# Kernel tuning notes

Hardware: AMD Instinct MI355X
Metric: run time of the kernel (lower is better)

## Reference

```python
import jax, jax.numpy as jnp
import numpy as np

B, J, D, W, H, EH, L = 128, 8192, 32, 4, 128, 256, 32
TEMP = 1.0


def _ln(x, g, b, eps=1e-5):
    mu = jnp.mean(x, axis=-1, keepdims=True)
    var = jnp.var(x, axis=-1, keepdims=True)
    return (x - mu) * jax.lax.rsqrt(var + eps) * g + b


def setup_inputs() -> dict:
    key = jax.random.key(0)
    ks = jax.random.split(key, 12)

    def lin(k, fi, fo):
        k1, k2 = jax.random.split(k)
        s = 1.0 / np.sqrt(fi)
        return (jax.random.uniform(k1, (fi, fo), minval=-s, maxval=s, dtype=jnp.float32),
                jax.random.uniform(k2, (fo,), minval=-s, maxval=s, dtype=jnp.float32))

    h_w1, h_b1 = lin(ks[0], 1 + D, H)
    h_w2, h_b2 = lin(ks[1], H, D)
    g_w1, g_b1 = lin(ks[2], D, D // 2)
    g_w2, g_b2 = lin(ks[3], D // 2, W)
    c_w, c_b = lin(ks[4], W * D, D)
    e_w1, e_b1 = lin(ks[5], D, EH)
    e_w2, e_b2 = lin(ks[6], EH, 2 * L)
    return {
        'x': jax.random.normal(ks[7], (B, J), dtype=jnp.float32),
        'mask': jax.random.randint(ks[8], (B, J), 0, 2, dtype=jnp.int32),
        'fe': jax.random.normal(ks[9], (J, D), dtype=jnp.float32),
        'h_w1': h_w1, 'h_b1': h_b1,
        'h_ln1_w': jnp.ones((H,), jnp.float32), 'h_ln1_b': jnp.zeros((H,), jnp.float32),
        'h_w2': h_w2, 'h_b2': h_b2,
        'h_ln2_w': jnp.ones((D,), jnp.float32), 'h_ln2_b': jnp.zeros((D,), jnp.float32),
        'g_w1': g_w1, 'g_b1': g_b1, 'g_w2': g_w2, 'g_b2': g_b2,
        'c_w': c_w, 'c_b': c_b,
        'c_ln_w': jnp.ones((D,), jnp.float32), 'c_ln_b': jnp.zeros((D,), jnp.float32),
        'e_w1': e_w1, 'e_b1': e_b1,
        'e_ln1_w': jnp.ones((EH,), jnp.float32), 'e_ln1_b': jnp.zeros((EH,), jnp.float32),
        'e_w2': e_w2, 'e_b2': e_b2,
        'e_ln2_w': jnp.ones((2 * L,), jnp.float32), 'e_ln2_b': jnp.zeros((2 * L,), jnp.float32),
    }


def _forward(x, mask, fe, h_w1, h_b1, h_ln1_w, h_ln1_b, h_w2, h_b2, h_ln2_w, h_ln2_b,
             g_w1, g_b1, g_w2, g_b2, c_w, c_b, c_ln_w, c_ln_b,
             e_w1, e_b1, e_ln1_w, e_ln1_b, e_w2, e_b2, e_ln2_w, e_ln2_b):
    relu = jax.nn.relu
    # h_in = concat([x, F]) @ h_w1 split into scalar column + shared embedding part
    # (fe @ h_w1[1:]) is [J,H], shared across cells -> avoids materializing [B,J,1+D]
    pre = x[..., None] * h_w1[0][None, None, :] + (fe @ h_w1[1:])[None] + h_b1  # [B,J,H]
    h1 = relu(_ln(pre, h_ln1_w, h_ln1_b))
    h_out = relu(_ln(h1 @ h_w2 + h_b2, h_ln2_w, h_ln2_b))  # [B,J,D]
    raw_gates = relu(h_out @ g_w1 + g_b1) @ g_w2 + g_b2  # [B,J,W]
    logits = jnp.clip(raw_gates * TEMP, -10.0, 10.0)
    logits = jnp.where(mask[..., None] > 0, logits, -1e9)  # masked gather -> -inf fill
    weights = jax.nn.softmax(logits, axis=1)  # softmax over observed junctions
    head_sums = jnp.einsum('bjw,bjd->bwd', weights, h_out)  # [B,W,D]
    comb = relu(_ln(head_sums.reshape(head_sums.shape[0], -1) @ c_w + c_b, c_ln_w, c_ln_b))
    comb = jnp.where((jnp.sum(mask, axis=1) > 0)[:, None], comb, 0.0)  # zero cells -> zeros
    h = relu(_ln(comb @ e_w1 + e_b1, e_ln1_w, e_ln1_b))
    o = relu(_ln(h @ e_w2 + e_b2, e_ln2_w, e_ln2_b))
    mu, logvar = jnp.split(o, 2, axis=-1)
    return mu, logvar


def reference(x, mask, fe, h_w1, h_b1, h_ln1_w, h_ln1_b, h_w2, h_b2, h_ln2_w, h_ln2_b,
              g_w1, g_b1, g_w2, g_b2, c_w, c_b, c_ln_w, c_ln_b,
              e_w1, e_b1, e_ln1_w, e_ln1_b, e_w2, e_b2, e_ln2_w, e_ln2_b):
    return _forward(x, mask, fe, h_w1, h_b1, h_ln1_w, h_ln1_b, h_w2, h_b2, h_ln2_w, h_ln2_b,
                    g_w1, g_b1, g_w2, g_b2, c_w, c_b, c_ln_w, c_ln_b,
                    e_w1, e_b1, e_ln1_w, e_ln1_b, e_w2, e_b2, e_ln2_w, e_ln2_b)
```

## Files before the change

kernel.cpp:

```cpp
#include <hip/hip_runtime.h>
#include <cstdint>

#define BDIM 128
#define JDIM 8192

typedef short s8x __attribute__((ext_vector_type(8)));
typedef float f4x __attribute__((ext_vector_type(4)));

__device__ __forceinline__ unsigned int rne16(float f) {
    unsigned int u = __float_as_uint(f);
    return (u + 0x7fffu + ((u >> 16) & 1u)) >> 16;
}
__device__ __forceinline__ unsigned int pkbf(float lo, float hi) {
    return rne16(lo) | (rne16(hi) << 16);
}
__device__ __forceinline__ float bf2f(unsigned int s) {
    return __uint_as_float(s << 16);
}

template <int CTRL>
__device__ __forceinline__ float dppadd(float x) {
    int y = __builtin_amdgcn_update_dpp(0, __builtin_bit_cast(int, x), CTRL, 0xF, 0xF, true);
    return x + __builtin_bit_cast(float, y);
}
__device__ __forceinline__ float allred16(float x) {
    x = dppadd<0xB1>(x);
    x = dppadd<0x4E>(x);
    x = dppadd<0x141>(x);
    x = dppadd<0x140>(x);
    return x;
}

__global__ __launch_bounds__(128) void k_prep(
    const float* __restrict__ fe, const float* __restrict__ hw1,
    const float* __restrict__ hb1,
    unsigned short* __restrict__ feWb, float* __restrict__ aux,
    float* __restrict__ scal)
{
    const int j = blockIdx.x, h = threadIdx.x;
    float acc = hb1[h];
#pragma unroll
    for (int d = 0; d < 32; ++d)
        acc = fmaf(fe[j * 32 + d], hw1[(1 + d) * 128 + h], acc);
    feWb[(size_t)j * 128 + h] = (unsigned short)rne16(acc);

    const float w0h = hw1[h];
    float s1 = acc, sx = w0h * acc, s2 = acc * acc;
#pragma unroll
    for (int m = 1; m <= 32; m <<= 1) {
        s1 += __shfl_xor(s1, m); sx += __shfl_xor(sx, m); s2 += __shfl_xor(s2, m);
    }
    __shared__ float red[2][3];
    const int wv = threadIdx.x >> 6, ln = threadIdx.x & 63;
    if (ln == 0) { red[wv][0] = s1; red[wv][1] = sx; red[wv][2] = s2; }
    __syncthreads();
    if (threadIdx.x == 0) {
        aux[j * 4 + 0] = (red[0][0] + red[1][0]) * (1.f / 128.f);
        aux[j * 4 + 1] = (red[0][1] + red[1][1]) * (1.f / 128.f);
        aux[j * 4 + 2] = (red[0][2] + red[1][2]) * (1.f / 128.f);
    }
    if (j == 0) {
        float a = w0h, b = w0h * w0h;
#pragma unroll
        for (int m = 1; m <= 32; m <<= 1) { a += __shfl_xor(a, m); b += __shfl_xor(b, m); }
        __syncthreads();
        if (ln == 0) { red[wv][0] = a; red[wv][1] = b; }
        __syncthreads();
        if (threadIdx.x == 0) {
            scal[0] = (red[0][0] + red[1][0]) * (1.f / 128.f);
            scal[1] = (red[0][1] + red[1][1]) * (1.f / 128.f);
        }
    }
}

__global__ __launch_bounds__(256, 2) void k_main(
    const float* __restrict__ x, const int* __restrict__ mask,
    const unsigned short* __restrict__ feWb, const float* __restrict__ aux,
    const float* __restrict__ scal,
    const float* __restrict__ hw1, const float* __restrict__ ln1w,
    const float* __restrict__ ln1b,
    const float* __restrict__ hw2, const float* __restrict__ hb2,
    const float* __restrict__ ln2w, const float* __restrict__ ln2b,
    const float* __restrict__ gw1, const float* __restrict__ gb1,
    const float* __restrict__ gw2, const float* __restrict__ gb2,
    float* __restrict__ P, float* __restrict__ SEb, int njb, int jpw)
{
    __shared__ float w0s[128], g1s[128], b1s[128];
    __shared__ float holds[8][576];
    __shared__ float hsL[2048];
    __shared__ float seL[64];

    const int tid = threadIdx.x, l = tid & 63;
    const int wv = __builtin_amdgcn_readfirstlane(tid >> 6);
    const int c = l & 15, g = l >> 4;
    const int bt = blockIdx.y, bx = blockIdx.x;
    const int b0 = bt * 16;

    if (tid < 128) { w0s[tid] = hw1[tid]; g1s[tid] = ln1w[tid]; b1s[tid] = ln1b[tid]; }
    __syncthreads();

    const float mw0 = scal[0], q0 = scal[1];

    s8x wf[2][4];
#pragma unroll
    for (int nt = 0; nt < 2; ++nt)
#pragma unroll
        for (int t = 0; t < 4; ++t) {
            const int kb = 32 * t + 8 * g, n = 16 * nt + c;
            uint4 u;
            u.x = pkbf(hw2[(kb + 0) * 32 + n], hw2[(kb + 1) * 32 + n]);
            u.y = pkbf(hw2[(kb + 2) * 32 + n], hw2[(kb + 3) * 32 + n]);
            u.z = pkbf(hw2[(kb + 4) * 32 + n], hw2[(kb + 5) * 32 + n]);
            u.w = pkbf(hw2[(kb + 6) * 32 + n], hw2[(kb + 7) * 32 + n]);
            wf[nt][t] = __builtin_bit_cast(s8x, u);
        }
    s8x g1f;
    {
        uint4 u;
        u.x = pkbf(gw1[(8 * g + 0) * 16 + c], gw1[(8 * g + 1) * 16 + c]);
        u.y = pkbf(gw1[(8 * g + 2) * 16 + c], gw1[(8 * g + 3) * 16 + c]);
        u.z = pkbf(gw1[(8 * g + 4) * 16 + c], gw1[(8 * g + 5) * 16 + c]);
        u.w = pkbf(gw1[(8 * g + 6) * 16 + c], gw1[(8 * g + 7) * 16 + c]);
        g1f = __builtin_bit_cast(s8x, u);
    }
    const float hb2a = hb2[c],      hb2b = hb2[16 + c];
    const float g2a  = ln2w[c],     g2b  = ln2w[16 + c];
    const float z2a  = ln2b[c],     z2b  = ln2b[16 + c];
    const float gb1c = gb1[c];
    float gw2c[4], gb2v[4];
#pragma unroll
    for (int w = 0; w < 4; ++w) { gw2c[w] = gw2[c * 4 + w]; gb2v[w] = gb2[w]; }

    const int j0 = (bx * 4 + wv) * jpw;
    const float* xrow = x + (size_t)(b0 + c) * JDIM;
    const int*   mrow = mask + (size_t)(b0 + c) * JDIM;

    float hsacc[4][4][2];
    float seacc[4][4];
#pragma unroll
    for (int r = 0; r < 4; ++r)
#pragma unroll
        for (int w = 0; w < 4; ++w) {
            hsacc[r][w][0] = 0.f; hsacc[r][w][1] = 0.f; seacc[r][w] = 0.f;
        }

    for (int jj = 0; jj < jpw; ++jj) {
        const int j = j0 + jj;
        const float xv = xrow[j];
        const int   mv = mrow[j];
        const float4 au = *(const float4*)(aux + j * 4);
        const float m1 = au.x, qx = au.y, q2 = au.z;
        const float mu = fmaf(xv, mw0, m1);
        const float e2 = fmaf(xv * xv, q0, fmaf(2.f * xv, qx, q2));
        const float rs = rsqrtf(e2 - mu * mu + 1e-5f);
        const float nms = -mu * rs;

        f4x ca = {0.f, 0.f, 0.f, 0.f}, cbv = {0.f, 0.f, 0.f, 0.f};
        const unsigned short* fj = feWb + (size_t)j * 128;
#pragma unroll
        for (int t = 0; t < 4; ++t) {
            const int kb = 32 * t + 8 * g;
            const uint4 fw = *(const uint4*)(fj + kb);
            const float pf0 = bf2f(fw.x & 0xffffu), pf1 = bf2f(fw.x >> 16);
            const float pf2 = bf2f(fw.y & 0xffffu), pf3 = bf2f(fw.y >> 16);
            const float pf4 = bf2f(fw.z & 0xffffu), pf5 = bf2f(fw.z >> 16);
            const float pf6 = bf2f(fw.w & 0xffffu), pf7 = bf2f(fw.w >> 16);
            const float4 wa = *(const float4*)&w0s[kb];
            const float4 wb = *(const float4*)&w0s[kb + 4];
            const float4 ga = *(const float4*)&g1s[kb];
            const float4 gbq = *(const float4*)&g1s[kb + 4];
            const float4 ba = *(const float4*)&b1s[kb];
            const float4 bb = *(const float4*)&b1s[kb + 4];
            const float h0 = fmaxf(fmaf(fmaf(fmaf(xv, wa.x, pf0), rs, nms), ga.x,  ba.x), 0.f);
            const float h1 = fmaxf(fmaf(fmaf(fmaf(xv, wa.y, pf1), rs, nms), ga.y,  ba.y), 0.f);
            const float h2 = fmaxf(fmaf(fmaf(fmaf(xv, wa.z, pf2), rs, nms), ga.z,  ba.z), 0.f);
            const float h3 = fmaxf(fmaf(fmaf(fmaf(xv, wa.w, pf3), rs, nms), ga.w,  ba.w), 0.f);
            const float h4 = fmaxf(fmaf(fmaf(fmaf(xv, wb.x, pf4), rs, nms), gbq.x, bb.x), 0.f);
            const float h5 = fmaxf(fmaf(fmaf(fmaf(xv, wb.y, pf5), rs, nms), gbq.y, bb.y), 0.f);
            const float h6 = fmaxf(fmaf(fmaf(fmaf(xv, wb.z, pf6), rs, nms), gbq.z, bb.z), 0.f);
            const float h7 = fmaxf(fmaf(fmaf(fmaf(xv, wb.w, pf7), rs, nms), gbq.w, bb.w), 0.f);
            uint4 u;
            u.x = pkbf(h0, h1); u.y = pkbf(h2, h3); u.z = pkbf(h4, h5); u.w = pkbf(h6, h7);
            const s8x af = __builtin_bit_cast(s8x, u);
            ca  = __builtin_amdgcn_mfma_f32_16x16x32_bf16(af, wf[0][t], ca,  0, 0, 0);
            cbv = __builtin_amdgcn_mfma_f32_16x16x32_bf16(af, wf[1][t], cbv, 0, 0, 0);
        }

        float v0[4], v1[4], sr[4], qr[4];
#pragma unroll
        for (int r = 0; r < 4; ++r) {
            v0[r] = ca[r] + hb2a;
            v1[r] = cbv[r] + hb2b;
            sr[r] = v0[r] + v1[r];
            qr[r] = v0[r] * v0[r] + v1[r] * v1[r];
        }
#pragma unroll
        for (int r = 0; r < 4; ++r) { sr[r] = allred16(sr[r]); qr[r] = allred16(qr[r]); }
        float ho0[4], ho1[4];
#pragma unroll
        for (int r = 0; r < 4; ++r) {
            const float m2  = sr[r] * 0.03125f;
            const float rs2 = rsqrtf(fmaf(qr[r], 0.03125f, -m2 * m2) + 1e-5f);
            const float nm2 = -m2 * rs2;
            ho0[r] = fmaxf(fmaf(fmaf(v0[r], rs2, nm2), g2a, z2a), 0.f);
            ho1[r] = fmaxf(fmaf(fmaf(v1[r], rs2, nm2), g2b, z2b), 0.f);
        }

        float* hp = &holds[wv * 2 + (jj & 1)][0];
#pragma unroll
        for (int r = 0; r < 4; ++r) {
            hp[(4 * g + r) * 36 + c]      = ho0[r];
            hp[(4 * g + r) * 36 + 16 + c] = ho1[r];
        }
        asm volatile("s_waitcnt lgkmcnt(0)" ::: "memory");
        const float4 ra  = *(const float4*)&hp[c * 36 + 8 * g];
        const float4 rb2 = *(const float4*)&hp[c * 36 + 8 * g + 4];
        uint4 ua;
        ua.x = pkbf(ra.x, ra.y);  ua.y = pkbf(ra.z, ra.w);
        ua.z = pkbf(rb2.x, rb2.y); ua.w = pkbf(rb2.z, rb2.w);
        const s8x af2 = __builtin_bit_cast(s8x, ua);
        f4x gc = {0.f, 0.f, 0.f, 0.f};
        gc = __builtin_amdgcn_mfma_f32_16x16x32_bf16(af2, g1f, gc, 0, 0, 0);

        float pw[16];
#pragma unroll
        for (int r = 0; r < 4; ++r) {
            const float g1r = fmaxf(gc[r] + gb1c, 0.f);
#pragma unroll
            for (int w = 0; w < 4; ++w) pw[r * 4 + w] = g1r * gw2c[w];
        }
#pragma unroll
        for (int i = 0; i < 16; ++i) pw[i] = allred16(pw[i]);

        const unsigned bm = (unsigned)__ballot(mv > 0);
        float fm[4];
#pragma unroll
        for (int r = 0; r < 4; ++r) fm[r] = (float)((bm >> (4 * g + r)) & 1u);

#pragma unroll
        for (int r = 0; r < 4; ++r)
#pragma unroll
            for (int w = 0; w < 4; ++w) {
                const float lg = fminf(fmaxf(pw[r * 4 + w] + gb2v[w], -10.f), 10.f);
                const float e  = fm[r] * __builtin_amdgcn_exp2f(
                                     fmaf(lg, 1.44269504089f, -14.4269504089f));
                seacc[r][w] += e;
                hsacc[r][w][0] = fmaf(e, ho0[r], hsacc[r][w][0]);
                hsacc[r][w][1] = fmaf(e, ho1[r], hsacc[r][w][1]);
            }
    }

    for (int ww = 0; ww < 4; ++ww) {
        __syncthreads();
        if (wv == ww) {
#pragma unroll
            for (int r = 0; r < 4; ++r)
#pragma unroll
                for (int w = 0; w < 4; ++w)
#pragma unroll
                    for (int nt = 0; nt < 2; ++nt) {
                        const int idx = ((4 * g + r) * 4 + w) * 32 + c + 16 * nt;
                        if (ww == 0) hsL[idx] = hsacc[r][w][nt];
                        else         hsL[idx] += hsacc[r][w][nt];
                    }
            if (c == 0) {
#pragma unroll
                for (int r = 0; r < 4; ++r)
#pragma unroll
                    for (int w = 0; w < 4; ++w) {
                        const int si = (4 * g + r) * 4 + w;
                        if (ww == 0) seL[si] = seacc[r][w];
                        else         seL[si] += seacc[r][w];
                    }
            }
        }
    }
    __syncthreads();
    const size_t base = ((size_t)bt * njb + bx) * 2048;
    for (int i = tid; i < 2048; i += 256) P[base + i] = hsL[i];
    if (tid < 64) SEb[((size_t)bt * njb + bx) * 64 + tid] = seL[tid];
}

__global__ __launch_bounds__(128) void k_tail(
    const float* __restrict__ P, const float* __restrict__ SEb,
    const float* __restrict__ cw, const float* __restrict__ cbv,
    const float* __restrict__ clnw, const float* __restrict__ clnb,
    const float* __restrict__ ew1, const float* __restrict__ eb1,
    const float* __restrict__ l1w, const float* __restrict__ l1b,
    const float* __restrict__ ew2, const float* __restrict__ eb2,
    const float* __restrict__ l2w, const float* __restrict__ l2b,
    float* __restrict__ out, int njb)
{
    const int b = blockIdx.x, t = threadIdx.x;
    const int bt = b >> 4, bi = b & 15;
    __shared__ float hsLs[128], combL[32], hL[256], seW[4], sred[64], red[4];

    const float* Pb = P + (size_t)bt * njb * 2048 + bi * 128;
    float sacc = 0.f;
#pragma unroll 4
    for (int jc = 0; jc < njb; ++jc) sacc += Pb[(size_t)jc * 2048 + t];

    if (t < 64) {
        const int w = t & 3, part = t >> 2;
        float sp = 0.f;
        for (int q = part; q < njb; q += 16)
            sp += SEb[((size_t)bt * njb + q) * 64 + bi * 4 + w];
        sred[t] = sp;
    }
    __syncthreads();
    if (t < 4) {
        float v = 0.f;
#pragma unroll
        for (int sl = 0; sl < 16; ++sl) v += sred[sl * 4 + t];
        seW[t] = v;
    }
    __syncthreads();
    const bool has = seW[0] > 0.f;
    hsLs[t] = has ? sacc / seW[t >> 5] : 0.f;
    __syncthreads();

    if (t < 32) {
        float cv = cbv[t];
#pragma unroll 4
        for (int f = 0; f < 128; ++f) cv = fmaf(hsLs[f], cw[f * 32 + t], cv);
        float s = cv, q = cv * cv;
#pragma unroll
        for (int m = 1; m <= 16; m <<= 1) { s += __shfl_xor(s, m); q += __shfl_xor(q, m); }
        const float mu = s * (1.f / 32.f);
        const float rsg = rsqrtf(fmaf(q, 1.f / 32.f, -mu * mu) + 1e-5f);
        const float v = fmaf(fmaf(cv, rsg, -mu * rsg), clnw[t], clnb[t]);
        combL[t] = has ? fmaxf(v, 0.f) : 0.f;
    }
    __syncthreads();

    float h0 = eb1[t], h1v = eb1[t + 128];
#pragma unroll 4
    for (int d = 0; d < 32; ++d) {
        const float cd = combL[d];
        h0  = fmaf(cd, ew1[d * 256 + t], h0);
        h1v = fmaf(cd, ew1[d * 256 + t + 128], h1v);
    }
    {
        float s = h0 + h1v, q = h0 * h0 + h1v * h1v;
#pragma unroll
        for (int m = 1; m <= 32; m <<= 1) { s += __shfl_xor(s, m); q += __shfl_xor(q, m); }
        const int wv = t >> 6, ln = t & 63;
        if (ln == 0) { red[wv * 2] = s; red[wv * 2 + 1] = q; }
    }
    __syncthreads();
    {
        const float S = red[0] + red[2], Q = red[1] + red[3];
        const float mu1 = S * (1.f / 256.f);
        const float rs1 = rsqrtf(fmaf(Q, 1.f / 256.f, -mu1 * mu1) + 1e-5f);
        hL[t]       = fmaxf(fmaf(fmaf(h0,  rs1, -mu1 * rs1), l1w[t],       l1b[t]),       0.f);
        hL[t + 128] = fmaxf(fmaf(fmaf(h1v, rs1, -mu1 * rs1), l1w[t + 128], l1b[t + 128]), 0.f);
    }
    __syncthreads();

    if (t < 64) {
        float ov = eb2[t];
#pragma unroll 4
        for (int m = 0; m < 256; ++m) ov = fmaf(hL[m], ew2[m * 64 + t], ov);
        float s = ov, q = ov * ov;
#pragma unroll
        for (int m = 1; m <= 32; m <<= 1) { s += __shfl_xor(s, m); q += __shfl_xor(q, m); }
        const float mu2 = s * (1.f / 64.f);
        const float rs2 = rsqrtf(fmaf(q, 1.f / 64.f, -mu2 * mu2) + 1e-5f);
        const float o = fmaxf(fmaf(fmaf(ov, rs2, -mu2 * rs2), l2w[t], l2b[t]), 0.f);
        if (t < 32) out[b * 32 + t] = o;
        else        out[4096 + b * 32 + (t - 32)] = o;
    }
}

extern "C" void kernel_launch(void* const* d_in, const int* in_sizes, int n_in,
                              void* d_out, int out_size, void* d_ws, size_t ws_size,
                              hipStream_t stream)
{
    (void)in_sizes; (void)n_in; (void)out_size;
    const float* x    = (const float*)d_in[0];
    const int*   mask = (const int*)d_in[1];
    const float* fe   = (const float*)d_in[2];
    const float* hw1  = (const float*)d_in[3];
    const float* hb1  = (const float*)d_in[4];
    const float* ln1w = (const float*)d_in[5];
    const float* ln1b = (const float*)d_in[6];
    const float* hw2  = (const float*)d_in[7];
    const float* hb2  = (const float*)d_in[8];
    const float* ln2w = (const float*)d_in[9];
    const float* ln2b = (const float*)d_in[10];
    const float* gw1  = (const float*)d_in[11];
    const float* gb1  = (const float*)d_in[12];
    const float* gw2  = (const float*)d_in[13];
    const float* gb2  = (const float*)d_in[14];
    const float* cw   = (const float*)d_in[15];
    const float* cbv  = (const float*)d_in[16];
    const float* clnw = (const float*)d_in[17];
    const float* clnb = (const float*)d_in[18];
    const float* ew1  = (const float*)d_in[19];
    const float* eb1  = (const float*)d_in[20];
    const float* l1w  = (const float*)d_in[21];
    const float* l1b  = (const float*)d_in[22];
    const float* ew2  = (const float*)d_in[23];
    const float* eb2  = (const float*)d_in[24];
    const float* l2w  = (const float*)d_in[25];
    const float* l2b  = (const float*)d_in[26];

    const size_t base = (2u << 20) + (128u << 10) + 256u;
    int NJB = 128;
    {
        const size_t need = base + (size_t)8 * 128 * 2048 * 4 + (size_t)8 * 128 * 64 * 4;
        if (ws_size < need) NJB = 64;
    }
    const int JPW = JDIM / (NJB * 4);

    char* ws = (char*)d_ws;
    unsigned short* feWb = (unsigned short*)ws;
    float* aux  = (float*)(ws + (2u << 20));
    float* scal = (float*)(ws + (2u << 20) + (128u << 10));
    float* P    = (float*)(ws + base);
    float* SEb  = (float*)(ws + base + (size_t)8 * NJB * 2048 * 4);

    hipLaunchKernelGGL(k_prep, dim3(JDIM), dim3(128), 0, stream,
                       fe, hw1, hb1, feWb, aux, scal);
    hipLaunchKernelGGL(k_main, dim3(NJB, 8), dim3(256), 0, stream,
                       x, mask, feWb, aux, scal,
                       hw1, ln1w, ln1b, hw2, hb2, ln2w, ln2b,
                       gw1, gb1, gw2, gb2, P, SEb, NJB, JPW);
    hipLaunchKernelGGL(k_tail, dim3(BDIM), dim3(128), 0, stream,
                       P, SEb, cw, cbv, clnw, clnb,
                       ew1, eb1, l1w, l1b, ew2, eb2, l2w, l2b,
                       (float*)d_out, NJB);
}
```

Baseline: 256.3 us.

## Use LDS atomics for cross-wave reduction, raise J-block count, and use hardware bf16 conversion

Replaces the serialized four-step wave-by-wave LDS accumulation with zero-initialized shared buffers and LDS atomicAdd, which removes three barriers. It also swaps the manual round-to-nearest bf16 conversion for the compiler's __bf16 cast, and replaces the fmin/fmax clamp with fmed3. NJB grows to 256 when the workspace allows, doubling the grid, and the tail kernel's partial-sum loop unrolls further. The extra blocks mean more partials for k_tail to reduce, and the atomic accumulation can contend on LDS.

```diff
diff --git a/kernel.cpp b/kernel.cpp
--- a/kernel.cpp
+++ b/kernel.cpp
@@ -7,12 +7,11 @@
 typedef short s8x __attribute__((ext_vector_type(8)));
 typedef float f4x __attribute__((ext_vector_type(4)));
 
-__device__ __forceinline__ unsigned int rne16(float f) {
-    unsigned int u = __float_as_uint(f);
-    return (u + 0x7fffu + ((u >> 16) & 1u)) >> 16;
+__device__ __forceinline__ unsigned short bf16u(float f) {
+    return __builtin_bit_cast(unsigned short, (__bf16)f);
 }
 __device__ __forceinline__ unsigned int pkbf(float lo, float hi) {
-    return rne16(lo) | (rne16(hi) << 16);
+    return (unsigned int)bf16u(lo) | ((unsigned int)bf16u(hi) << 16);
 }
 __device__ __forceinline__ float bf2f(unsigned int s) {
     return __uint_as_float(s << 16);
@@ -42,7 +41,7 @@
 #pragma unroll
     for (int d = 0; d < 32; ++d)
         acc = fmaf(fe[j * 32 + d], hw1[(1 + d) * 128 + h], acc);
-    feWb[(size_t)j * 128 + h] = (unsigned short)rne16(acc);
+    feWb[(size_t)j * 128 + h] = bf16u(acc);
 
     const float w0h = hw1[h];
     float s1 = acc, sx = w0h * acc, s2 = acc * acc;
@@ -97,6 +96,8 @@
     const int b0 = bt * 16;
 
     if (tid < 128) { w0s[tid] = hw1[tid]; g1s[tid] = ln1w[tid]; b1s[tid] = ln1b[tid]; }
+    for (int i = tid; i < 2048; i += 256) hsL[i] = 0.f;
+    if (tid < 64) seL[tid] = 0.f;
     __syncthreads();
 
     const float mw0 = scal[0], q0 = scal[1];
@@ -241,7 +242,7 @@
         for (int r = 0; r < 4; ++r)
 #pragma unroll
             for (int w = 0; w < 4; ++w) {
-                const float lg = fminf(fmaxf(pw[r * 4 + w] + gb2v[w], -10.f), 10.f);
+                const float lg = __builtin_amdgcn_fmed3f(pw[r * 4 + w] + gb2v[w], -10.f, 10.f);
                 const float e  = fm[r] * __builtin_amdgcn_exp2f(
                                      fmaf(lg, 1.44269504089f, -14.4269504089f));
                 seacc[r][w] += e;
@@ -250,31 +251,18 @@
             }
     }
 
-    for (int ww = 0; ww < 4; ++ww) {
-        __syncthreads();
-        if (wv == ww) {
-#pragma unroll
-            for (int r = 0; r < 4; ++r)
-#pragma unroll
-                for (int w = 0; w < 4; ++w)
-#pragma unroll
-                    for (int nt = 0; nt < 2; ++nt) {
-                        const int idx = ((4 * g + r) * 4 + w) * 32 + c + 16 * nt;
-                        if (ww == 0) hsL[idx] = hsacc[r][w][nt];
-                        else         hsL[idx] += hsacc[r][w][nt];
-                    }
-            if (c == 0) {
-#pragma unroll
-                for (int r = 0; r < 4; ++r)
-#pragma unroll
-                    for (int w = 0; w < 4; ++w) {
-                        const int si = (4 * g + r) * 4 + w;
-                        if (ww == 0) seL[si] = seacc[r][w];
-                        else         seL[si] += seacc[r][w];
-                    }
+    __syncthreads();
+#pragma unroll
+    for (int r = 0; r < 4; ++r)
+#pragma unroll
+        for (int w = 0; w < 4; ++w) {
+#pragma unroll
+            for (int nt = 0; nt < 2; ++nt) {
+                const int idx = ((4 * g + r) * 4 + w) * 32 + c + 16 * nt;
+                atomicAdd(&hsL[idx], hsacc[r][w][nt]);
             }
-        }
-    }
+            if (c == 0) atomicAdd(&seL[(4 * g + r) * 4 + w], seacc[r][w]);
+        }
     __syncthreads();
     const size_t base = ((size_t)bt * njb + bx) * 2048;
     for (int i = tid; i < 2048; i += 256) P[base + i] = hsL[i];
@@ -297,7 +285,7 @@
 
     const float* Pb = P + (size_t)bt * njb * 2048 + bi * 128;
     float sacc = 0.f;
-#pragma unroll 4
+#pragma unroll 8
     for (int jc = 0; jc < njb; ++jc) sacc += Pb[(size_t)jc * 2048 + t];
 
     if (t < 64) {
@@ -406,10 +394,11 @@
     const float* l2b  = (const float*)d_in[26];
 
     const size_t base = (2u << 20) + (128u << 10) + 256u;
-    int NJB = 128;
-    {
-        const size_t need = base + (size_t)8 * 128 * 2048 * 4 + (size_t)8 * 128 * 64 * 4;
-        if (ws_size < need) NJB = 64;
+    int NJB = 256;
+    while (NJB > 64) {
+        const size_t need = base + (size_t)8 * NJB * 2048 * 4 + (size_t)8 * NJB * 64 * 4;
+        if (ws_size >= need) break;
+        NJB >>= 1;
     }
     const int JPW = JDIM / (NJB * 4);
 
```

After: 334.3 us. 1.3x slower.
